# Performance work log

Hardware: AMD Instinct MI355X
Metric: run time of the kernel (lower is better)

The kernel has to match this reference:

```python
import jax, jax.numpy as jnp
import numpy as np


def setup_inputs() -> dict:
    key = jax.random.key(0)
    k1, k2 = jax.random.split(key)
    B, C = 65536, 1000
    output = jax.random.normal(k1, (B, C), dtype=jnp.float32)
    target = jax.random.uniform(k2, (B, C), dtype=jnp.float32)  # soft labels in [0,1)
    return {"output": output, "target": target}


def _multivector_ce(output, target, size_average=True):
    # For each row: positives P = {t>0.5}, negatives N = {t<=0.5}.
    # Original loop computes, per positive p:
    #   loss_p = sum_{j in N u {p}} -t_j * log_softmax_{N u {p}}(o)_j
    # which factors through shared negative-set statistics:
    #   LSE_p = log( sum_{j in N} exp(o_j) + exp(o_p) )
    #   loss_p = (Tneg + t_p) * LSE_p - Aneg - t_p * o_p
    # with Tneg = sum_N t_j, Aneg = sum_N t_j * o_j.
    neg = target <= 0.5                                   # [B, C] bool
    m = jnp.max(output, axis=1, keepdims=True)            # [B, 1] stability shift
    e = jnp.exp(output - m)                               # [B, C]
    zero = jnp.zeros((), dtype=output.dtype)
    Sneg = jnp.sum(jnp.where(neg, e, zero), axis=1, keepdims=True)              # [B, 1]
    Tneg = jnp.sum(jnp.where(neg, target, zero), axis=1, keepdims=True)         # [B, 1]
    Aneg = jnp.sum(jnp.where(neg, target * output, zero), axis=1, keepdims=True)

    lse_p = m + jnp.log(Sneg + e)                         # [B, C], LSE of N u {p} per candidate p
    loss_p = (Tneg + target) * lse_p - Aneg - target * output   # [B, C]

    pos = ~neg
    n_pos = jnp.sum(pos, axis=1)                          # [B] int
    pos_loss = jnp.sum(jnp.where(pos, loss_p, zero), axis=1)    # [B]

    # Fallback when a row has no positives: loss over negatives only.
    lse_neg = (m + jnp.log(Sneg))[:, 0]                   # [B]
    fallback = Tneg[:, 0] * lse_neg - Aneg[:, 0]          # [B]

    denom = jnp.maximum(n_pos, 1).astype(output.dtype)
    row_loss = jnp.where(n_pos > 0, pos_loss / denom, fallback)  # [B]

    total = jnp.sum(row_loss)
    if size_average:
        return total / output.shape[0]
    return total


def reference(output, target):
    return _multivector_ce(output, target, size_average=True)
```

## Files before the change

### kernel.cpp

```cpp
#include <hip/hip_runtime.h>
#include <math.h>

#define C_DIM 1000
#define NV4   (C_DIM / 4)
#define WPB   4
#define RPW   4
#define PAD_O (-100.0f)

__device__ __forceinline__ float wave_sum(float v) {
#pragma unroll
    for (int off = 32; off > 0; off >>= 1)
        v += __shfl_xor(v, off, 64);
    return v;
}

__global__ __launch_bounds__(256) void mvce_rows(
    const float* __restrict__ outp, const float* __restrict__ tgtp,
    float* __restrict__ partial)
{
    const int lane  = threadIdx.x & 63;
    const int wave  = threadIdx.x >> 6;
    const int wgid  = blockIdx.x * WPB + wave;

    float wsum = 0.0f;

#pragma unroll
    for (int r = 0; r < RPW; ++r) {
        const int row = wgid * RPW + r;
        const float4* orow = reinterpret_cast<const float4*>(outp + (size_t)row * C_DIM);
        const float4* trow = reinterpret_cast<const float4*>(tgtp + (size_t)row * C_DIM);

        float o[16], t[16];
#pragma unroll
        for (int it = 0; it < 4; ++it) {
            const int j = lane + 64 * it;
            if (j < NV4) {
                const float4 ov = orow[j];
                const float4 tv = trow[j];
                o[4 * it + 0] = ov.x; o[4 * it + 1] = ov.y;
                o[4 * it + 2] = ov.z; o[4 * it + 3] = ov.w;
                t[4 * it + 0] = tv.x; t[4 * it + 1] = tv.y;
                t[4 * it + 2] = tv.z; t[4 * it + 3] = tv.w;
            } else {
#pragma unroll
                for (int q = 0; q < 4; ++q) {
                    o[4 * it + q] = PAD_O;
                    t[4 * it + q] = 0.0f;
                }
            }
        }

        float S[4] = {0.f, 0.f, 0.f, 0.f};
        float T[4] = {0.f, 0.f, 0.f, 0.f};
        float A[4] = {0.f, 0.f, 0.f, 0.f};
        float P[4] = {0.f, 0.f, 0.f, 0.f};
#pragma unroll
        for (int k = 0; k < 16; ++k) {
            const int a = k & 3;
            const float e  = __expf(o[k]);
            const bool neg = (t[k] <= 0.5f);
            const float tn = neg ? t[k] : 0.0f;
            S[a] += neg ? e : 0.0f;
            T[a] += tn;
            A[a]  = fmaf(tn, o[k], A[a]);
            P[a] += neg ? 0.0f : 1.0f;
        }
        float Sneg = wave_sum((S[0] + S[1]) + (S[2] + S[3]));
        float Tneg = wave_sum((T[0] + T[1]) + (T[2] + T[3]));
        float Aneg = wave_sum((A[0] + A[1]) + (A[2] + A[3]));
        float nposf = wave_sum((P[0] + P[1]) + (P[2] + P[3]));

        float L[4] = {0.f, 0.f, 0.f, 0.f};
#pragma unroll
        for (int k = 0; k < 16; ++k) {
            const int a = k & 3;
            const float e   = __expf(o[k]);
            const float lse = __logf(Sneg + e);
            const float b   = fmaf(t[k], o[k], Aneg);
            const float c   = fmaf(Tneg + t[k], lse, -b);
            L[a] += (t[k] > 0.5f) ? c : 0.0f;
        }
        float lsum = wave_sum((L[0] + L[1]) + (L[2] + L[3]));

        float row_loss;
        if (nposf > 0.5f) row_loss = lsum / nposf;
        else              row_loss = fmaf(Tneg, __logf(Sneg), -Aneg);
        wsum += row_loss;
    }

    __shared__ float ls[WPB];
    if (lane == 0) ls[wave] = wsum;
    __syncthreads();
    if (threadIdx.x == 0)
        partial[blockIdx.x] = (ls[0] + ls[1]) + (ls[2] + ls[3]);
}

__global__ __launch_bounds__(256) void mvce_reduce(
    const float* __restrict__ partial, int n4, float inv_b, float* __restrict__ out)
{
    const float4* p4 = reinterpret_cast<const float4*>(partial);
    float s = 0.f;
#pragma unroll 4
    for (int i = threadIdx.x; i < n4; i += 256) {
        const float4 v = p4[i];
        s += (v.x + v.y) + (v.z + v.w);
    }
    s = wave_sum(s);
    __shared__ float ls[4];
    const int lane = threadIdx.x & 63;
    const int wave = threadIdx.x >> 6;
    if (lane == 0) ls[wave] = s;
    __syncthreads();
    if (threadIdx.x == 0) out[0] = ((ls[0] + ls[1]) + (ls[2] + ls[3])) * inv_b;
}

extern "C" void kernel_launch(void* const* d_in, const int* in_sizes, int n_in,
                              void* d_out, int out_size, void* d_ws, size_t ws_size,
                              hipStream_t stream) {
    const float* outp = (const float*)d_in[0];
    const float* tgtp = (const float*)d_in[1];
    const int Bn = in_sizes[0] / C_DIM;
    const int nblocks = Bn / (WPB * RPW);
    float* partial = (float*)d_ws;

    mvce_rows<<<nblocks, 256, 0, stream>>>(outp, tgtp, partial);
    mvce_reduce<<<1, 256, 0, stream>>>(partial, nblocks / 4, 1.0f / (float)Bn,
                                       (float*)d_out);
}
```

Before: 498.6 us.

## Prefetch next row, batch wave reductions, reuse exp, defer loss reduction

Software-pipelines row loads by fetching row r+1 into a second register set while row r is computed, so memory latency can overlap with compute. The four statistic reductions are interleaved into one shuffle loop, exp values are cached instead of recomputed, and the per-row loss reduction is postponed to a single wave_sum at the end by dividing each lane's partial by the row's positive count. This costs more registers, which may lower occupancy, and the deferred sum changes the floating-point summation order.

Result: no change. 495.1 us (-0.7%).

```diff
diff --git a/kernel.cpp b/kernel.cpp
--- a/kernel.cpp
+++ b/kernel.cpp
@@ -14,79 +14,98 @@
     return v;
 }
 
+__device__ __forceinline__ void wave_sum4(float& a, float& b, float& c, float& d) {
+#pragma unroll
+    for (int off = 32; off > 0; off >>= 1) {
+        const float ax = __shfl_xor(a, off, 64);
+        const float bx = __shfl_xor(b, off, 64);
+        const float cx = __shfl_xor(c, off, 64);
+        const float dx = __shfl_xor(d, off, 64);
+        a += ax; b += bx; c += cx; d += dx;
+    }
+}
+
+__device__ __forceinline__ void load_row(
+    const float* __restrict__ outp, const float* __restrict__ tgtp,
+    int row, int lane, float o[16], float t[16])
+{
+    const float4* orow = reinterpret_cast<const float4*>(outp + (size_t)row * C_DIM);
+    const float4* trow = reinterpret_cast<const float4*>(tgtp + (size_t)row * C_DIM);
+#pragma unroll
+    for (int it = 0; it < 4; ++it) {
+        const int j = lane + 64 * it;
+        if (j < NV4) {
+            const float4 ov = orow[j];
+            const float4 tv = trow[j];
+            o[4 * it + 0] = ov.x; o[4 * it + 1] = ov.y;
+            o[4 * it + 2] = ov.z; o[4 * it + 3] = ov.w;
+            t[4 * it + 0] = tv.x; t[4 * it + 1] = tv.y;
+            t[4 * it + 2] = tv.z; t[4 * it + 3] = tv.w;
+        } else {
+#pragma unroll
+            for (int q = 0; q < 4; ++q) {
+                o[4 * it + q] = PAD_O;
+                t[4 * it + q] = 0.0f;
+            }
+        }
+    }
+}
+
 __global__ __launch_bounds__(256) void mvce_rows(
     const float* __restrict__ outp, const float* __restrict__ tgtp,
     float* __restrict__ partial)
 {
-    const int lane  = threadIdx.x & 63;
-    const int wave  = threadIdx.x >> 6;
-    const int wgid  = blockIdx.x * WPB + wave;
+    const int lane = threadIdx.x & 63;
+    const int wave = threadIdx.x >> 6;
+    const int wgid = blockIdx.x * WPB + wave;
+    const int row0 = wgid * RPW;
 
-    float wsum = 0.0f;
+    float oA[16], tA[16], oB[16], tB[16];
+    load_row(outp, tgtp, row0, lane, oA, tA);
+
+    float wsum_lane = 0.0f;
 
 #pragma unroll
     for (int r = 0; r < RPW; ++r) {
-        const int row = wgid * RPW + r;
-        const float4* orow = reinterpret_cast<const float4*>(outp + (size_t)row * C_DIM);
-        const float4* trow = reinterpret_cast<const float4*>(tgtp + (size_t)row * C_DIM);
+        if (r + 1 < RPW)
+            load_row(outp, tgtp, row0 + r + 1, lane, oB, tB);
 
-        float o[16], t[16];
+        float e[16];
+        float S = 0.f, T = 0.f, A = 0.f, P = 0.f;
 #pragma unroll
-        for (int it = 0; it < 4; ++it) {
-            const int j = lane + 64 * it;
-            if (j < NV4) {
-                const float4 ov = orow[j];
-                const float4 tv = trow[j];
-                o[4 * it + 0] = ov.x; o[4 * it + 1] = ov.y;
-                o[4 * it + 2] = ov.z; o[4 * it + 3] = ov.w;
-                t[4 * it + 0] = tv.x; t[4 * it + 1] = tv.y;
-                t[4 * it + 2] = tv.z; t[4 * it + 3] = tv.w;
-            } else {
+        for (int k = 0; k < 16; ++k) {
+            e[k] = __expf(oA[k]);
+            const bool neg = (tA[k] <= 0.5f);
+            const float tn = neg ? tA[k] : 0.0f;
+            S += neg ? e[k] : 0.0f;
+            T += tn;
+            A  = fmaf(tn, oA[k], A);
+            P += neg ? 0.0f : 1.0f;
+        }
+        wave_sum4(S, T, A, P);
+
+        float L = 0.f;
 #pragma unroll
-                for (int q = 0; q < 4; ++q) {
-                    o[4 * it + q] = PAD_O;
-                    t[4 * it + q] = 0.0f;
-                }
-            }
+        for (int k = 0; k < 16; ++k) {
+            const float lse = __logf(S + e[k]);
+            const float b   = fmaf(tA[k], oA[k], A);
+            const float c   = fmaf(T + tA[k], lse, -b);
+            L += (tA[k] > 0.5f) ? c : 0.0f;
         }
 
-        float S[4] = {0.f, 0.f, 0.f, 0.f};
-        float T[4] = {0.f, 0.f, 0.f, 0.f};
-        float A[4] = {0.f, 0.f, 0.f, 0.f};
-        float P[4] = {0.f, 0.f, 0.f, 0.f};
+        if (P > 0.5f) {
+            wsum_lane += L / P;
+        } else if (lane == 0) {
+            wsum_lane += fmaf(T, __logf(S), -A);
+        }
+
+        if (r + 1 < RPW) {
 #pragma unroll
-        for (int k = 0; k < 16; ++k) {
-            const int a = k & 3;
-            const float e  = __expf(o[k]);
-            const bool neg = (t[k] <= 0.5f);
-            const float tn = neg ? t[k] : 0.0f;
-            S[a] += neg ? e : 0.0f;
-            T[a] += tn;
-            A[a]  = fmaf(tn, o[k], A[a]);
-            P[a] += neg ? 0.0f : 1.0f;
+            for (int k = 0; k < 16; ++k) { oA[k] = oB[k]; tA[k] = tB[k]; }
         }
-        float Sneg = wave_sum((S[0] + S[1]) + (S[2] + S[3]));
-        float Tneg = wave_sum((T[0] + T[1]) + (T[2] + T[3]));
-        float Aneg = wave_sum((A[0] + A[1]) + (A[2] + A[3]));
-        float nposf = wave_sum((P[0] + P[1]) + (P[2] + P[3]));
+    }
 
-        float L[4] = {0.f, 0.f, 0.f, 0.f};
-#pragma unroll
-        for (int k = 0; k < 16; ++k) {
-            const int a = k & 3;
-            const float e   = __expf(o[k]);
-            const float lse = __logf(Sneg + e);
-            const float b   = fmaf(t[k], o[k], Aneg);
-            const float c   = fmaf(Tneg + t[k], lse, -b);
-            L[a] += (t[k] > 0.5f) ? c : 0.0f;
-        }
-        float lsum = wave_sum((L[0] + L[1]) + (L[2] + L[3]));
-
-        float row_loss;
-        if (nposf > 0.5f) row_loss = lsum / nposf;
-        else              row_loss = fmaf(Tneg, __logf(Sneg), -Aneg);
-        wsum += row_loss;
-    }
+    const float wsum = wave_sum(wsum_lane);
 
     __shared__ float ls[WPB];
     if (lane == 0) ls[wave] = wsum;
```
